# Optimization experiments

Hardware: AMD Instinct MI355X
Metric: run time of the kernel (lower is better)

## Reference

```python
import jax, jax.numpy as jnp
import numpy as np

EMBED_DIM = 256
HEADS = 8
HEAD_DIM = EMBED_DIM // HEADS
T = 8            # time grid points
N0, N1 = 32, 32  # spatial grid
MAX_PATCH = 16   # static slot budget per cell (last slot = grid latent token)
NEG = -1e30


def construct_grid():
    g0 = jnp.linspace(0.0, 1.0, N0)
    g1 = jnp.linspace(0.0, 1.0, N1)
    G0, G1 = jnp.meshgrid(g0, g1, indexing='ij')
    return jnp.stack([G0, G1], axis=-1)  # [N0, N1, 2]


def setup_inputs() -> dict:
    key = jax.random.key(0)
    ks = jax.random.split(key, 8)
    m, n = 4, 16384
    x = jax.random.uniform(ks[0], (m, n, 3))                       # coords: (time, s0, s1) in [0,1]
    z = jax.random.normal(ks[1], (m, n, EMBED_DIM))
    time_grid = jnp.tile(jnp.linspace(0.0, 1.0, T)[None], (m, 1))  # [m, T] uniform time grid
    latents = jax.random.normal(ks[2], (N0, N1, EMBED_DIM))
    grid = construct_grid()
    s = 1.0 / np.sqrt(EMBED_DIM)
    Wq = jax.random.normal(ks[3], (EMBED_DIM, EMBED_DIM)) * s
    Wk = jax.random.normal(ks[4], (EMBED_DIM, EMBED_DIM)) * s
    Wv = jax.random.normal(ks[5], (EMBED_DIM, EMBED_DIM)) * s
    Wo = jax.random.normal(ks[6], (EMBED_DIM, EMBED_DIM)) * s
    return {'x': x, 'z': z, 'time_grid': time_grid, 'latents': latents,
            'grid': grid, 'Wq': Wq, 'Wk': Wk, 'Wv': Wv, 'Wo': Wo}


def _cumcount(idx):
    # idx: [n] int; returns per-element count of prior occurrences of the same value
    n = idx.shape[0]
    order = jnp.argsort(idx)                 # stable
    srt = idx[order]
    ar = jnp.arange(n)
    is_start = jnp.concatenate([jnp.array([True]), srt[1:] != srt[:-1]])
    seg_start = jax.lax.cummax(jnp.where(is_start, ar, 0), axis=0)
    cc = ar - seg_start
    return jnp.zeros_like(idx).at[order].set(cc.astype(idx.dtype))


def _forward(x, z, time_grid, latents, grid, Wq, Wk, Wv, Wo):
    m, n, _ = x.shape
    t = time_grid.shape[1]
    S = t * N0 * N1
    # --- build x_grid: repeat spatial grid over (m,t), insert time coord at dim 0 ---
    xg_sp = jnp.broadcast_to(grid[None, None], (m, t, N0, N1, 2))
    tg = jnp.broadcast_to(time_grid[:, :, None, None, None], (m, t, N0, N1, 1))
    x_grid = jnp.concatenate([tg, xg_sp], axis=-1)          # [m,t,N0,N1,3]
    # --- nearest gridded neighbour (k=1): per-dim rounding on the regular grid ---
    grid_shape = jnp.array([t, N0, N1], jnp.float32)
    xg_flat = x_grid.reshape(m, S, 3)
    xmin = xg_flat.min(axis=1)                               # [m,3]
    xmax = xg_flat.max(axis=1)
    spacing = (xmax - xmin) / (grid_shape - 1.0)             # [m,3]
    multi = jnp.floor((x - xmin[:, None] + spacing[:, None] / 2) / spacing[:, None])
    multi = jnp.clip(multi, 0.0, grid_shape - 1.0)
    strides = jnp.array([N0 * N1, N1, 1], jnp.float32)
    nearest = jnp.sum(multi * strides, axis=-1).astype(jnp.int32)  # [m,n] flat cell id
    # --- per-cell slot allocation via cumulative count ---
    cum = jax.vmap(_cumcount)(nearest)                       # [m,n]
    P = MAX_PATCH
    valid = cum < (P - 1)                                    # last slot reserved for grid token
    bidx = jnp.arange(m)[:, None]
    cell = jnp.where(valid, nearest, S)                      # out-of-bounds -> dropped
    slot = jnp.minimum(cum, P - 2)
    # --- scatter points into the joint grid [m, S, P, E]; slot P-1 = grid latent ---
    joint = jnp.zeros((m, S, P, EMBED_DIM), z.dtype)
    joint = joint.at[bidx, cell, slot].set(z, mode='drop')
    z_grid_flat = jnp.broadcast_to(
        latents.reshape(1, 1, N0 * N1, EMBED_DIM), (m, t, N0 * N1, EMBED_DIM)
    ).reshape(m, S, EMBED_DIM)
    joint = joint.at[:, :, P - 1].set(z_grid_flat)
    counts = jnp.zeros((m, S), jnp.int32).at[bidx, cell].add(1, mode='drop')
    counts = jnp.minimum(counts, P - 1)
    att_mask = jnp.concatenate(
        [jnp.arange(P - 1)[None, None] < counts[..., None],
         jnp.ones((m, S, 1), bool)], axis=-1)                # [m,S,P]
    # --- masked multi-head cross attention: 1 query (grid latent) per cell ---
    q = (z_grid_flat @ Wq).reshape(m, S, HEADS, HEAD_DIM)
    k = (joint @ Wk).reshape(m, S, P, HEADS, HEAD_DIM)
    v = (joint @ Wv).reshape(m, S, P, HEADS, HEAD_DIM)
    logits = jnp.einsum('mshd,msphd->mshp', q, k) / np.sqrt(HEAD_DIM)
    logits = jnp.where(att_mask[:, :, None, :], logits, NEG)
    attn = jax.nn.softmax(logits, axis=-1)
    out = jnp.einsum('mshp,msphd->mshd', attn, v).reshape(m, S, EMBED_DIM) @ Wo
    z_grid = out.reshape(m, t, N0, N1, EMBED_DIM)
    return x_grid, z_grid


def reference(x, z, time_grid, latents, grid, Wq, Wk, Wv, Wo):
    return _forward(x, z, time_grid, latents, grid, Wq, Wk, Wv, Wo)
```

## Files before the change

### kernel.cpp

```cpp
#include <hip/hip_runtime.h>
#include <hip/hip_bf16.h>

#define T_ 8
#define N0_ 32
#define N1_ 32
#define SP_ (N0_*N1_)
#define S_ (T_*SP_)
#define E_ 256
#define P_ 16
#define NH_ 8
#define HD_ 32

typedef __attribute__((ext_vector_type(8))) short short8;
typedef __attribute__((ext_vector_type(4))) float f32x4;
typedef __attribute__((ext_vector_type(8))) unsigned short u16x8;

__device__ __forceinline__ unsigned short f2bf(float f) {
  __hip_bfloat16 h = __float2bfloat16(f);
  return *reinterpret_cast<unsigned short*>(&h);
}
__device__ __forceinline__ float bf2f(unsigned short u) {
  return __uint_as_float((unsigned)u << 16);
}

__device__ __forceinline__ void gl_lds16(const void* g, void* l) {
  __builtin_amdgcn_global_load_lds(
      (const __attribute__((address_space(1))) unsigned int*)(g),
      (__attribute__((address_space(3))) unsigned int*)(l), 16, 0, 0);
}

__global__ __launch_bounds__(256) void prep(const float* __restrict__ z,
                                            unsigned short* __restrict__ z16,
                                            const float* __restrict__ x,
                                            const float* __restrict__ tg,
                                            const float* __restrict__ grid,
                                            float* __restrict__ out,
                                            int* __restrict__ counts,
                                            int* __restrict__ cell_raw,
                                            const float* __restrict__ Wq,
                                            const float* __restrict__ Wk,
                                            const float* __restrict__ Wv,
                                            const float* __restrict__ Wo,
                                            unsigned short* __restrict__ wT,
                                            const float* __restrict__ latents,
                                            unsigned short* __restrict__ lat16,
                                            int m, int n, int tot_xg, int zn8) {
  __shared__ float ts[64][65];
  __shared__ float st[4][6];
  int bid = blockIdx.x;
  int tid = threadIdx.x;
  if (bid < 2048) {
    for (int i = bid * 256 + tid; i < zn8; i += 2048 * 256) {
      float4 a = *(const float4*)(z + (size_t)i * 8);
      float4 b = *(const float4*)(z + (size_t)i * 8 + 4);
      u16x8 o;
      o[0]=f2bf(a.x); o[1]=f2bf(a.y); o[2]=f2bf(a.z); o[3]=f2bf(a.w);
      o[4]=f2bf(b.x); o[5]=f2bf(b.y); o[6]=f2bf(b.z); o[7]=f2bf(b.w);
      *(u16x8*)(z16 + (size_t)i * 8) = o;
    }
    return;
  }
  if (bid < 2304) {
    if (tid < 64) {
      float mn0 = 1e30f, mx0 = -1e30f, mn1 = 1e30f, mx1 = -1e30f;
      for (int i = tid; i < SP_; i += 64) {
        float g0 = grid[i*2], g1 = grid[i*2+1];
        mn0 = fminf(mn0, g0); mx0 = fmaxf(mx0, g0);
        mn1 = fminf(mn1, g1); mx1 = fmaxf(mx1, g1);
      }
      for (int msk = 32; msk; msk >>= 1) {
        mn0 = fminf(mn0, __shfl_xor(mn0, msk));
        mx0 = fmaxf(mx0, __shfl_xor(mx0, msk));
        mn1 = fminf(mn1, __shfl_xor(mn1, msk));
        mx1 = fmaxf(mx1, __shfl_xor(mx1, msk));
      }
      if (tid == 0) {
        for (int b = 0; b < m; ++b) {
          float tmn = 1e30f, tmx = -1e30f;
          for (int tt = 0; tt < T_; ++tt) {
            float v = tg[b*T_ + tt];
            tmn = fminf(tmn, v); tmx = fmaxf(tmx, v);
          }
          st[b][0] = tmn; st[b][1] = mn0; st[b][2] = mn1;
          st[b][3] = (tmx - tmn) / (float)(T_ - 1);
          st[b][4] = (mx0 - mn0) / (float)(N0_ - 1);
          st[b][5] = (mx1 - mn1) / (float)(N1_ - 1);
        }
      }
    }
    __syncthreads();
    int idx = (bid - 2048) * 256 + tid;
    if (idx < tot_xg) {
      int sp = idx & (SP_ - 1);
      int bt = idx >> 10;
      out[idx*3 + 0] = tg[bt];
      out[idx*3 + 1] = grid[sp*2 + 0];
      out[idx*3 + 2] = grid[sp*2 + 1];
    }
    if (idx < m*n) {
      int b = idx / n;
      int j = idx - b*n;
      const float* s = st[b];
      float xt = x[(size_t)idx*3 + 0], x0 = x[(size_t)idx*3 + 1], x1 = x[(size_t)idx*3 + 2];
      float m0 = floorf((xt - s[0] + s[3]*0.5f) / s[3]);
      float m1 = floorf((x0 - s[1] + s[4]*0.5f) / s[4]);
      float m2 = floorf((x1 - s[2] + s[5]*0.5f) / s[5]);
      m0 = fminf(fmaxf(m0, 0.f), (float)(T_ - 1));
      m1 = fminf(fmaxf(m1, 0.f), (float)(N0_ - 1));
      m2 = fminf(fmaxf(m2, 0.f), (float)(N1_ - 1));
      int sc = (int)m0 * SP_ + (int)m1 * N1_ + (int)m2;
      int cg = b * S_ + sc;
      int old = atomicAdd(&counts[cg], 1);
      if (old < P_) cell_raw[(size_t)cg * P_ + old] = j;
    }
    return;
  }
  if (bid < 2368) {
    int wb = bid - 2304;
    int mat = wb >> 4;
    int tile = wb & 15;
    int tr = (tile >> 2) * 64;
    int tc = (tile & 3) * 64;
    const float* W = mat == 0 ? Wq : mat == 1 ? Wk : mat == 2 ? Wv : Wo;
    int r = tid >> 2, c0 = (tid & 3) * 16;
#pragma unroll
    for (int i = 0; i < 4; ++i) {
      float4 v = *(const float4*)&W[(size_t)(tr + r) * 256 + tc + c0 + i*4];
      ts[r][c0 + i*4 + 0] = v.x; ts[r][c0 + i*4 + 1] = v.y;
      ts[r][c0 + i*4 + 2] = v.z; ts[r][c0 + i*4 + 3] = v.w;
    }
    __syncthreads();
    u16x8 o0, o1;
#pragma unroll
    for (int i = 0; i < 8; ++i) o0[i] = f2bf(ts[c0 + i][r]);
#pragma unroll
    for (int i = 0; i < 8; ++i) o1[i] = f2bf(ts[c0 + 8 + i][r]);
    unsigned short* dst = wT + (size_t)(mat * 256 + tc + r) * 256 + tr + c0;
    *(u16x8*)dst = o0;
    *(u16x8*)(dst + 8) = o1;
    return;
  }
  for (int i = (bid - 2368) * 256 + tid; i < SP_ * E_ / 8; i += 16 * 256) {
    float4 a = *(const float4*)(latents + (size_t)i * 8);
    float4 b = *(const float4*)(latents + (size_t)i * 8 + 4);
    u16x8 o;
    o[0]=f2bf(a.x); o[1]=f2bf(a.y); o[2]=f2bf(a.z); o[3]=f2bf(a.w);
    o[4]=f2bf(b.x); o[5]=f2bf(b.y); o[6]=f2bf(b.z); o[7]=f2bf(b.w);
    *(u16x8*)(lat16 + (size_t)i * 8) = o;
  }
}

template <typename OutT>
__device__ __forceinline__ void g2l_body(unsigned short* __restrict__ ldsbuf,
                                         const unsigned short* __restrict__ A,
                                         const unsigned short* __restrict__ BT,
                                         OutT* __restrict__ C,
                                         int CP, int ldc, int L, int tid) {
  int rp = L / CP, cp = L - rp * CP;

  int wid = tid >> 6, lane = tid & 63, l15 = lane & 15, slot = lane >> 4;
  int wr = (wid >> 2) * 64, wc = (wid & 3) * 32;

  int r8 = lane >> 3, k8 = lane & 7;
  int colsw = (k8 ^ r8) << 3;
  const unsigned short* ga0 = A  + (size_t)(rp * 128 + wid * 16 + r8) * 256 + colsw;
  const unsigned short* gb0 = BT + (size_t)(cp * 128 + wid * 16 + r8) * 256 + colsw;

#define STAGE(b, kt) do { \
    const unsigned short* ga = ga0 + (kt) * 64; \
    const unsigned short* gb = gb0 + (kt) * 64; \
    gl_lds16(ga,         ldsbuf + ((b)*2    ) * 8192 + (wid*16    ) * 64); \
    gl_lds16(ga + 8*256, ldsbuf + ((b)*2    ) * 8192 + (wid*16 + 8) * 64); \
    gl_lds16(gb,         ldsbuf + ((b)*2 + 1) * 8192 + (wid*16    ) * 64); \
    gl_lds16(gb + 8*256, ldsbuf + ((b)*2 + 1) * 8192 + (wid*16 + 8) * 64); \
  } while (0)

  f32x4 acc[4][2] = {};
  STAGE(0, 0);

#pragma unroll
  for (int kt = 0; kt < 4; ++kt) {
    int b = kt & 1;
    if (kt < 3) STAGE(b ^ 1, kt + 1);
    if (kt < 3) asm volatile("s_waitcnt vmcnt(4)" ::: "memory");
    else        asm volatile("s_waitcnt vmcnt(0)" ::: "memory");
    __builtin_amdgcn_s_barrier();
    asm volatile("" ::: "memory");
    const unsigned short* As = ldsbuf + (b*2) * 8192;
    const unsigned short* Bs = ldsbuf + (b*2 + 1) * 8192;
#pragma unroll
    for (int kf = 0; kf < 2; ++kf) {
      short8 afr[4], bfr[2];
      int kg = kf * 4 + slot;
      int sx = kg ^ (l15 & 7);
#pragma unroll
      for (int mm = 0; mm < 4; ++mm) {
        int row = wr + mm * 16 + l15;
        afr[mm] = *(const short8*)&As[row * 64 + (sx << 3)];
      }
#pragma unroll
      for (int nn = 0; nn < 2; ++nn) {
        int col = wc + nn * 16 + l15;
        bfr[nn] = *(const short8*)&Bs[col * 64 + (sx << 3)];
      }
#pragma unroll
      for (int mm = 0; mm < 4; ++mm)
#pragma unroll
        for (int nn = 0; nn < 2; ++nn)
          acc[mm][nn] = __builtin_amdgcn_mfma_f32_16x16x32_bf16(afr[mm], bfr[nn], acc[mm][nn], 0, 0, 0);
    }
    asm volatile("" ::: "memory");
    __builtin_amdgcn_s_barrier();
    asm volatile("" ::: "memory");
  }
#undef STAGE

#pragma unroll
  for (int mm = 0; mm < 4; ++mm) {
#pragma unroll
    for (int nn = 0; nn < 2; ++nn) {
      int grow0 = rp * 128 + wr + mm * 16 + slot * 4;
      int gcol  = cp * 128 + wc + nn * 16 + l15;
#pragma unroll
      for (int j = 0; j < 4; ++j) {
        size_t o = (size_t)(grow0 + j) * ldc + gcol;
        if constexpr (__is_same(OutT, float)) C[o] = acc[mm][nn][j];
        else                                  C[o] = __float2bfloat16(acc[mm][nn][j]);
      }
    }
  }
}

__global__ __launch_bounds__(512, 4) void phase2(const unsigned short* __restrict__ z16,
                                                 const unsigned short* __restrict__ wT,
                                                 __hip_bfloat16* __restrict__ kv,
                                                 const unsigned short* __restrict__ lat16,
                                                 float* __restrict__ lat,
                                                 const int* __restrict__ counts,
                                                 int* __restrict__ cell_raw,
                                                 int* __restrict__ pts2, int total) {
  __shared__ unsigned short lds[4 * 128 * 64];
  int bid = blockIdx.x;
  if (bid < 2048) {
    int L = (bid & 7) * 256 + (bid >> 3);
    g2l_body<__hip_bfloat16>(lds, z16, wT + (size_t)256*256, kv, 4, 512, L, threadIdx.x);
    return;
  }
  if (bid < 2096) {
    g2l_body<float>(lds, lat16, wT, lat, 6, 768, bid - 2048, threadIdx.x);
    return;
  }
  int cg = (bid - 2096) * 512 + threadIdx.x;
  if (cg >= total) return;
  int cnt = counts[cg];
  int stored = cnt < P_ ? cnt : P_;
  int eff = cnt < (P_ - 1) ? cnt : (P_ - 1);
  int* p = cell_raw + (size_t)cg * P_;
  for (int i = 1; i < stored; ++i) {
    int key = p[i]; int j = i - 1;
    while (j >= 0 && p[j] > key) { p[j+1] = p[j]; --j; }
    p[j+1] = key;
  }
  int* o = pts2 + (size_t)cg * P_;
  o[0] = eff;
  for (int i = 0; i < eff; ++i) o[1 + i] = p[i];
}

template <typename OutT>
__global__ __launch_bounds__(512, 4) void gemm_g2l(const unsigned short* __restrict__ A,
                                                   const unsigned short* __restrict__ BT,
                                                   OutT* __restrict__ C,
                                                   int CP, int ldc) {
  __shared__ unsigned short lds[4 * 128 * 64];
  int nb = gridDim.x, bid = blockIdx.x;
  int L = bid;
  if ((nb & 7) == 0) L = (bid & 7) * (nb >> 3) + (bid >> 3);
  g2l_body<OutT>(lds, A, BT, C, CP, ldc, L, threadIdx.x);
}

__global__ __launch_bounds__(256) void attn_kernel(
    const float* __restrict__ lat,
    const __hip_bfloat16* __restrict__ kv,
    const int* __restrict__ pts2,
    __hip_bfloat16* __restrict__ attn_out, int n) {
  const float scale = 0.17677669529663687f;
  int wid = threadIdx.x >> 6;
  int lane = threadIdx.x & 63;
  int cellg = blockIdx.x * 4 + wid;
  int b = cellg >> 13;
  int c = cellg & (SP_ - 1);
  int d0 = lane << 2;

  const int* pp = pts2 + (size_t)cellg * P_;
  int4 h0 = *(const int4*)pp;
  int eff = h0.x;

  const float* latc = lat + c * 768 + d0;
  float4 q  = *(const float4*)latc;
  float4 kl = *(const float4*)(latc + 256);
  float4 vl = *(const float4*)(latc + 512);

  float part = q.x*kl.x + q.y*kl.y + q.z*kl.z + q.w*kl.w;
  part += __shfl_xor(part, 1);
  part += __shfl_xor(part, 2);
  part += __shfl_xor(part, 4);
  float mx = part * scale;
  float ssum = 1.f;
  float4 acc = vl;

  const unsigned short* kvp = (const unsigned short*)kv;
  size_t bbase = (size_t)b * n;

  int pt[4]; pt[0] = h0.y; pt[1] = h0.z; pt[2] = h0.w; pt[3] = 0;
  int done = 0, cap = 3;
  while (done < eff) {
    int np = eff - done; if (np > cap) np = cap;
    ushort4 kr[4], vr[4];
#pragma unroll
    for (int i = 0; i < 4; ++i) if (i < np) {
      size_t row = (bbase + (size_t)pt[i]) * 512;
      kr[i] = *(const ushort4*)(kvp + row + d0);
      vr[i] = *(const ushort4*)(kvp + row + 256 + d0);
    }
#pragma unroll
    for (int i = 0; i < 4; ++i) if (i < np) {
      float p = q.x*bf2f(kr[i].x) + q.y*bf2f(kr[i].y) + q.z*bf2f(kr[i].z) + q.w*bf2f(kr[i].w);
      p += __shfl_xor(p, 1);
      p += __shfl_xor(p, 2);
      p += __shfl_xor(p, 4);
      p *= scale;
      float m2 = fmaxf(mx, p);
      float corr = __expf(mx - m2);
      float e = __expf(p - m2);
      ssum = ssum * corr + e;
      acc.x = acc.x * corr + e * bf2f(vr[i].x);
      acc.y = acc.y * corr + e * bf2f(vr[i].y);
      acc.z = acc.z * corr + e * bf2f(vr[i].z);
      acc.w = acc.w * corr + e * bf2f(vr[i].w);
      mx = m2;
    }
    done += np;
    cap = 4;
    if (done < eff) {
      int4 h = *(const int4*)(pp + 1 + done);
      pt[0] = h.x; pt[1] = h.y; pt[2] = h.z; pt[3] = h.w;
    }
  }
  float inv = 1.f / ssum;
  ushort4 o;
  o.x = f2bf(acc.x * inv); o.y = f2bf(acc.y * inv);
  o.z = f2bf(acc.z * inv); o.w = f2bf(acc.w * inv);
  *(ushort4*)((unsigned short*)attn_out + (size_t)cellg * E_ + d0) = o;
}

extern "C" void kernel_launch(void* const* d_in, const int* in_sizes, int n_in,
                              void* d_out, int out_size, void* d_ws, size_t ws_size,
                              hipStream_t stream) {
  const float* x       = (const float*)d_in[0];
  const float* z       = (const float*)d_in[1];
  const float* tg      = (const float*)d_in[2];
  const float* latents = (const float*)d_in[3];
  const float* grid    = (const float*)d_in[4];
  const float* Wq      = (const float*)d_in[5];
  const float* Wk      = (const float*)d_in[6];
  const float* Wv      = (const float*)d_in[7];
  const float* Wo      = (const float*)d_in[8];

  int m = in_sizes[2] / T_;
  int n = in_sizes[1] / (m * E_);
  int MS = m * S_;
  float* out = (float*)d_out;
  int tot_xg = m * T_ * SP_;

  char* w = (char*)d_ws;
  auto alloc = [&](size_t bytes) { char* p = w; w += (bytes + 255) & ~(size_t)255; return p; };
  int*   counts     = (int*)  alloc((size_t)MS * 4);
  int*   cell_raw   = (int*)  alloc((size_t)MS * P_ * 4);
  int*   pts2       = (int*)  alloc((size_t)MS * P_ * 4);
  unsigned short* wT    = (unsigned short*)alloc((size_t)1024 * 256 * 2);
  unsigned short* lat16 = (unsigned short*)alloc((size_t)SP_ * E_ * 2);
  float* lat        = (float*)alloc((size_t)SP_ * 768 * 4);
  __hip_bfloat16* kv       = (__hip_bfloat16*)alloc((size_t)m * n * 512 * 2);
  __hip_bfloat16* attn_out = (__hip_bfloat16*)alloc((size_t)MS * E_ * 2);

  unsigned short* z16 = (unsigned short*)(out + (size_t)tot_xg * 3);

  (void)hipMemsetAsync(counts, 0, (size_t)MS * 4, stream);

  prep<<<2384, 256, 0, stream>>>(z, z16, x, tg, grid, out, counts, cell_raw,
                                 Wq, Wk, Wv, Wo, wT, latents, lat16,
                                 m, n, tot_xg, m * n * E_ / 8);

  phase2<<<2160, 512, 0, stream>>>(z16, wT, kv, lat16, lat, counts, cell_raw, pts2, MS);

  attn_kernel<<<MS/4, 256, 0, stream>>>(lat, kv, pts2, attn_out, n);

  gemm_g2l<float><<<512, 512, 0, stream>>>(
      (const unsigned short*)attn_out, wT + (size_t)768*256, out + (size_t)tot_xg * 3, 2, 256);
}
```

Measured before the change: 98.64 us.

## Use 4-wave 64x64 warp tiles in GEMMs and drop online-softmax max tracking

```diff
diff --git a/kernel.cpp b/kernel.cpp
--- a/kernel.cpp
+++ b/kernel.cpp
@@ -159,30 +159,34 @@
   int rp = L / CP, cp = L - rp * CP;
 
   int wid = tid >> 6, lane = tid & 63, l15 = lane & 15, slot = lane >> 4;
-  int wr = (wid >> 2) * 64, wc = (wid & 3) * 32;
+  int wr = (wid >> 1) * 64, wc = (wid & 1) * 64;
 
   int r8 = lane >> 3, k8 = lane & 7;
   int colsw = (k8 ^ r8) << 3;
-  const unsigned short* ga0 = A  + (size_t)(rp * 128 + wid * 16 + r8) * 256 + colsw;
-  const unsigned short* gb0 = BT + (size_t)(cp * 128 + wid * 16 + r8) * 256 + colsw;
+  const unsigned short* ga0 = A  + (size_t)(rp * 128 + wid * 32 + r8) * 256 + colsw;
+  const unsigned short* gb0 = BT + (size_t)(cp * 128 + wid * 32 + r8) * 256 + colsw;
 
 #define STAGE(b, kt) do { \
     const unsigned short* ga = ga0 + (kt) * 64; \
     const unsigned short* gb = gb0 + (kt) * 64; \
-    gl_lds16(ga,         ldsbuf + ((b)*2    ) * 8192 + (wid*16    ) * 64); \
-    gl_lds16(ga + 8*256, ldsbuf + ((b)*2    ) * 8192 + (wid*16 + 8) * 64); \
-    gl_lds16(gb,         ldsbuf + ((b)*2 + 1) * 8192 + (wid*16    ) * 64); \
-    gl_lds16(gb + 8*256, ldsbuf + ((b)*2 + 1) * 8192 + (wid*16 + 8) * 64); \
+    gl_lds16(ga,          ldsbuf + ((b)*2    ) * 8192 + (wid*32     ) * 64); \
+    gl_lds16(ga +  8*256, ldsbuf + ((b)*2    ) * 8192 + (wid*32 +  8) * 64); \
+    gl_lds16(ga + 16*256, ldsbuf + ((b)*2    ) * 8192 + (wid*32 + 16) * 64); \
+    gl_lds16(ga + 24*256, ldsbuf + ((b)*2    ) * 8192 + (wid*32 + 24) * 64); \
+    gl_lds16(gb,          ldsbuf + ((b)*2 + 1) * 8192 + (wid*32     ) * 64); \
+    gl_lds16(gb +  8*256, ldsbuf + ((b)*2 + 1) * 8192 + (wid*32 +  8) * 64); \
+    gl_lds16(gb + 16*256, ldsbuf + ((b)*2 + 1) * 8192 + (wid*32 + 16) * 64); \
+    gl_lds16(gb + 24*256, ldsbuf + ((b)*2 + 1) * 8192 + (wid*32 + 24) * 64); \
   } while (0)
 
-  f32x4 acc[4][2] = {};
+  f32x4 acc[4][4] = {};
   STAGE(0, 0);
 
 #pragma unroll
   for (int kt = 0; kt < 4; ++kt) {
     int b = kt & 1;
     if (kt < 3) STAGE(b ^ 1, kt + 1);
-    if (kt < 3) asm volatile("s_waitcnt vmcnt(4)" ::: "memory");
+    if (kt < 3) asm volatile("s_waitcnt vmcnt(8)" ::: "memory");
     else        asm volatile("s_waitcnt vmcnt(0)" ::: "memory");
     __builtin_amdgcn_s_barrier();
     asm volatile("" ::: "memory");
@@ -190,23 +194,22 @@
     const unsigned short* Bs = ldsbuf + (b*2 + 1) * 8192;
 #pragma unroll
     for (int kf = 0; kf < 2; ++kf) {
-      short8 afr[4], bfr[2];
-      int kg = kf * 4 + slot;
-      int sx = kg ^ (l15 & 7);
+      short8 afr[4], bfr[4];
+      int sx = (kf * 4 + slot) ^ (l15 & 7);
 #pragma unroll
       for (int mm = 0; mm < 4; ++mm) {
         int row = wr + mm * 16 + l15;
         afr[mm] = *(const short8*)&As[row * 64 + (sx << 3)];
       }
 #pragma unroll
-      for (int nn = 0; nn < 2; ++nn) {
+      for (int nn = 0; nn < 4; ++nn) {
         int col = wc + nn * 16 + l15;
         bfr[nn] = *(const short8*)&Bs[col * 64 + (sx << 3)];
       }
 #pragma unroll
       for (int mm = 0; mm < 4; ++mm)
 #pragma unroll
-        for (int nn = 0; nn < 2; ++nn)
+        for (int nn = 0; nn < 4; ++nn)
           acc[mm][nn] = __builtin_amdgcn_mfma_f32_16x16x32_bf16(afr[mm], bfr[nn], acc[mm][nn], 0, 0, 0);
     }
     asm volatile("" ::: "memory");
@@ -218,7 +221,7 @@
 #pragma unroll
   for (int mm = 0; mm < 4; ++mm) {
 #pragma unroll
-    for (int nn = 0; nn < 2; ++nn) {
+    for (int nn = 0; nn < 4; ++nn) {
       int grow0 = rp * 128 + wr + mm * 16 + slot * 4;
       int gcol  = cp * 128 + wc + nn * 16 + l15;
 #pragma unroll
@@ -231,7 +234,7 @@
   }
 }
 
-__global__ __launch_bounds__(512, 4) void phase2(const unsigned short* __restrict__ z16,
+__global__ __launch_bounds__(256, 2) void phase2(const unsigned short* __restrict__ z16,
                                                  const unsigned short* __restrict__ wT,
                                                  __hip_bfloat16* __restrict__ kv,
                                                  const unsigned short* __restrict__ lat16,
@@ -250,7 +253,7 @@
     g2l_body<float>(lds, lat16, wT, lat, 6, 768, bid - 2048, threadIdx.x);
     return;
   }
-  int cg = (bid - 2096) * 512 + threadIdx.x;
+  int cg = (bid - 2096) * 256 + threadIdx.x;
   if (cg >= total) return;
   int cnt = counts[cg];
   int stored = cnt < P_ ? cnt : P_;
@@ -267,7 +270,7 @@
 }
 
 template <typename OutT>
-__global__ __launch_bounds__(512, 4) void gemm_g2l(const unsigned short* __restrict__ A,
+__global__ __launch_bounds__(256, 2) void gemm_g2l(const unsigned short* __restrict__ A,
                                                    const unsigned short* __restrict__ BT,
                                                    OutT* __restrict__ C,
                                                    int CP, int ldc) {
@@ -300,13 +303,14 @@
   float4 kl = *(const float4*)(latc + 256);
   float4 vl = *(const float4*)(latc + 512);
 
-  float part = q.x*kl.x + q.y*kl.y + q.z*kl.z + q.w*kl.w;
-  part += __shfl_xor(part, 1);
-  part += __shfl_xor(part, 2);
-  part += __shfl_xor(part, 4);
-  float mx = part * scale;
-  float ssum = 1.f;
-  float4 acc = vl;
+  float p15 = q.x*kl.x + q.y*kl.y + q.z*kl.z + q.w*kl.w;
+  p15 += __shfl_xor(p15, 1);
+  p15 += __shfl_xor(p15, 2);
+  p15 += __shfl_xor(p15, 4);
+  float e15 = __expf(p15 * scale);
+  float ssum = e15;
+  float4 acc;
+  acc.x = e15 * vl.x; acc.y = e15 * vl.y; acc.z = e15 * vl.z; acc.w = e15 * vl.w;
 
   const unsigned short* kvp = (const unsigned short*)kv;
   size_t bbase = (size_t)b * n;
@@ -322,22 +326,22 @@
       kr[i] = *(const ushort4*)(kvp + row + d0);
       vr[i] = *(const ushort4*)(kvp + row + 256 + d0);
     }
+    float e[4];
 #pragma unroll
     for (int i = 0; i < 4; ++i) if (i < np) {
       float p = q.x*bf2f(kr[i].x) + q.y*bf2f(kr[i].y) + q.z*bf2f(kr[i].z) + q.w*bf2f(kr[i].w);
       p += __shfl_xor(p, 1);
       p += __shfl_xor(p, 2);
       p += __shfl_xor(p, 4);
-      p *= scale;
-      float m2 = fmaxf(mx, p);
-      float corr = __expf(mx - m2);
-      float e = __expf(p - m2);
-      ssum = ssum * corr + e;
-      acc.x = acc.x * corr + e * bf2f(vr[i].x);
-      acc.y = acc.y * corr + e * bf2f(vr[i].y);
-      acc.z = acc.z * corr + e * bf2f(vr[i].z);
-      acc.w = acc.w * corr + e * bf2f(vr[i].w);
-      mx = m2;
+      e[i] = __expf(p * scale);
+    }
+#pragma unroll
+    for (int i = 0; i < 4; ++i) if (i < np) {
+      ssum += e[i];
+      acc.x += e[i] * bf2f(vr[i].x);
+      acc.y += e[i] * bf2f(vr[i].y);
+      acc.z += e[i] * bf2f(vr[i].z);
+      acc.w += e[i] * bf2f(vr[i].w);
     }
     done += np;
     cap = 4;
@@ -391,10 +395,10 @@
                                  Wq, Wk, Wv, Wo, wT, latents, lat16,
                                  m, n, tot_xg, m * n * E_ / 8);
 
-  phase2<<<2160, 512, 0, stream>>>(z16, wT, kv, lat16, lat, counts, cell_raw, pts2, MS);
+  phase2<<<2224, 256, 0, stream>>>(z16, wT, kv, lat16, lat, counts, cell_raw, pts2, MS);
 
   attn_kernel<<<MS/4, 256, 0, stream>>>(lat, kv, pts2, attn_out, n);
 
-  gemm_g2l<float><<<512, 512, 0, stream>>>(
+  gemm_g2l<float><<<512, 256, 0, stream>>>(
       (const unsigned short*)attn_out, wT + (size_t)768*256, out + (size_t)tot_xg * 3, 2, 256);
 }
```

Measured after the change: 92.34 us. 6.4% less time.
